# Performance work log

Measured on AMD Instinct MI355X. Metric: run time of the kernel, lower is better.

## Reference

```python
import jax, jax.numpy as jnp
import numpy as np

STATE_DIM = 150
HIDDEN = 64
ACTION_DIM = 10
TEAM = 5
PRED_STEPS = 5
HEADS = 4
BATCH = 16384


def _lin_params(key, out_dim, in_dim):
    kw, kb = jax.random.split(key)
    w = jax.random.normal(kw, (out_dim, in_dim), dtype=jnp.float32) * 0.05
    b = jax.random.normal(kb, (out_dim,), dtype=jnp.float32) * 0.05
    return w, b


def setup_inputs() -> dict:
    key = jax.random.key(0)
    ks = jax.random.split(key, 16)
    x = jax.random.normal(ks[0], (BATCH, STATE_DIM), dtype=jnp.float32)
    fc1_w, fc1_b = _lin_params(ks[1], HIDDEN, STATE_DIM)
    fc2_w, fc2_b = _lin_params(ks[2], HIDDEN, HIDDEN)
    fc3_w, fc3_b = _lin_params(ks[3], ACTION_DIM, HIDDEN)
    h0_w, h0_b = _lin_params(ks[4], HIDDEN, HIDDEN)
    c0_w, c0_b = _lin_params(ks[5], HIDDEN, HIDDEN)
    lstm_wih = jax.random.normal(ks[6], (4 * HIDDEN, HIDDEN), dtype=jnp.float32) * 0.05
    lstm_whh = jax.random.normal(ks[7], (4 * HIDDEN, HIDDEN), dtype=jnp.float32) * 0.05
    lstm_bih = jax.random.normal(ks[8], (4 * HIDDEN,), dtype=jnp.float32) * 0.05
    lstm_bhh = jax.random.normal(ks[9], (4 * HIDDEN,), dtype=jnp.float32) * 0.05
    predfc_w, predfc_b = _lin_params(ks[10], TEAM * STATE_DIM, HIDDEN)
    emb_w, emb_b = _lin_params(ks[11], HIDDEN, STATE_DIM)
    attn_in_w = jax.random.normal(ks[12], (3 * HIDDEN, HIDDEN), dtype=jnp.float32) * 0.05
    attn_in_b = jax.random.normal(ks[13], (3 * HIDDEN,), dtype=jnp.float32) * 0.05
    attn_out_w, attn_out_b = _lin_params(ks[14], HIDDEN, HIDDEN)
    unemb_w, unemb_b = _lin_params(ks[15], STATE_DIM, HIDDEN)
    return dict(x=x, fc1_w=fc1_w, fc1_b=fc1_b, fc2_w=fc2_w, fc2_b=fc2_b,
                fc3_w=fc3_w, fc3_b=fc3_b, h0_w=h0_w, h0_b=h0_b, c0_w=c0_w,
                c0_b=c0_b, lstm_wih=lstm_wih, lstm_whh=lstm_whh,
                lstm_bih=lstm_bih, lstm_bhh=lstm_bhh, predfc_w=predfc_w,
                predfc_b=predfc_b, emb_w=emb_w, emb_b=emb_b,
                attn_in_w=attn_in_w, attn_in_b=attn_in_b,
                attn_out_w=attn_out_w, attn_out_b=attn_out_b,
                unemb_w=unemb_w, unemb_b=unemb_b)


def _mha(x, in_w, in_b, out_w, out_b):
    # x: [B, S, E]; torch MultiheadAttention with batch_first=True, q=k=v=x
    B, S, E = x.shape
    D = E // HEADS
    qkv = x @ in_w.T + in_b                      # [B, S, 3E]
    q, k, v = jnp.split(qkv, 3, axis=-1)
    def heads(t):  # [B, S, E] -> [B, H, S, D]
        return t.reshape(B, S, HEADS, D).transpose(0, 2, 1, 3)
    q, k, v = heads(q), heads(k), heads(v)
    scores = jnp.einsum('bhqd,bhkd->bhqk', q, k) / jnp.sqrt(jnp.float32(D))
    attn = jax.nn.softmax(scores, axis=-1)
    out = jnp.einsum('bhqk,bhkd->bhqd', attn, v)  # [B, H, S, D]
    out = out.transpose(0, 2, 1, 3).reshape(B, S, E)
    return out @ out_w.T + out_b


def reference(x, fc1_w, fc1_b, fc2_w, fc2_b, fc3_w, fc3_b, h0_w, h0_b, c0_w,
              c0_b, lstm_wih, lstm_whh, lstm_bih, lstm_bhh, predfc_w,
              predfc_b, emb_w, emb_b, attn_in_w, attn_in_b, attn_out_w,
              attn_out_b, unemb_w, unemb_b):
    B = x.shape[0]
    h1 = jax.nn.relu(x @ fc1_w.T + fc1_b)
    h2 = jax.nn.relu(h1 @ fc2_w.T + fc2_b)
    action_probs = jax.nn.softmax(h2 @ fc3_w.T + fc3_b, axis=1)
    h = h2 @ h0_w.T + h0_b
    c = h2 @ c0_w.T + c0_b
    zero_in = jnp.zeros((B, HIDDEN), dtype=x.dtype)

    def step(carry, _):
        h, c = carry
        gates = zero_in @ lstm_wih.T + lstm_bih + h @ lstm_whh.T + lstm_bhh
        i, f, g, o = jnp.split(gates, 4, axis=-1)
        c_new = jax.nn.sigmoid(f) * c + jax.nn.sigmoid(i) * jnp.tanh(g)
        h_new = jax.nn.sigmoid(o) * jnp.tanh(c_new)
        pred_step = (h_new @ predfc_w.T + predfc_b).reshape(B, TEAM, STATE_DIM)
        embeds = pred_step @ emb_w.T + emb_b          # [B, TEAM, HIDDEN]
        att = _mha(embeds, attn_in_w, attn_in_b, attn_out_w, attn_out_b)
        out = att @ unemb_w.T + unemb_b               # [B, TEAM, STATE_DIM]
        return (h_new, c_new), out

    (_, _), preds = jax.lax.scan(step, (h, c), None, length=PRED_STEPS)
    pred = preds.transpose(1, 0, 2, 3)  # [B, PRED_STEPS, TEAM, STATE_DIM]
    return action_probs, pred
```

## Files before the change

kernel.cpp:

```cpp
#include <hip/hip_runtime.h>


#define RF(x) __builtin_amdgcn_readfirstlane(x)

constexpr int BATCH = 16384;

typedef short bf16x8 __attribute__((ext_vector_type(8)));
typedef float f32x4  __attribute__((ext_vector_type(4)));

constexpr int WS_FC1T = 0;
constexpr int WS_FC2T = 9728;
constexpr int WS_FC3T = 13824;
constexpr int WS_H0T  = 14592;
constexpr int WS_C0T  = 18688;
constexpr int WS_WHHT = 22784;
constexpr int WS_GB   = 39168;
constexpr int WS_W2   = 39424;
constexpr int WS_B2   = 59904;
constexpr int WS_W3QK = 60224;
constexpr int WS_W3V  = 101184;
constexpr int WS_B3QK = 121664;
constexpr int WS_B3V  = 122304;
constexpr int WS_W4T  = 122624;
constexpr int WS_B4   = 132352;
constexpr int WS_FC3B = 132504;
constexpr int WS_W4F  = 132520;
constexpr int WS_GF   = 142760;
constexpr int WS_VF   = 159144;
constexpr int WS_QKF  = 179624;
constexpr int WS_TOTAL= 220584;

constexpr int VSTR     = 324;
constexpr int QK_OFF   = 10368;
constexpr int QKSTR    = 164;
constexpr int H_OFF    = 15616;
constexpr int C_OFF    = 17792;
constexpr int HSTR     = 68;
constexpr int XSTR     = 156;
constexpr int H1_OFF   = QK_OFF;
constexpr int H2_OFF   = 4992;
constexpr int LDS_DW   = 19968;

__device__ __forceinline__ unsigned rnbf16_bits(float f) {
    unsigned u = __float_as_uint(f);
    return (u + 0x7FFFu + ((u >> 16) & 1u)) >> 16;
}

__global__ void k_pre1(const float* __restrict__ fc1_w, const float* __restrict__ fc2_w,
                       const float* __restrict__ fc3_w, const float* __restrict__ fc3_b,
                       const float* __restrict__ h0_w,  const float* __restrict__ c0_w,
                       const float* __restrict__ whh,   const float* __restrict__ bih,
                       const float* __restrict__ bhh,
                       const float* __restrict__ predfc_w, const float* __restrict__ predfc_b,
                       const float* __restrict__ emb_w,    const float* __restrict__ emb_b,
                       const float* __restrict__ aow, const float* __restrict__ aob,
                       const float* __restrict__ unw, const float* __restrict__ unb,
                       float* ws)
{
    int idx = blockIdx.x * 256 + threadIdx.x;
    if (idx < 9728) { int k = idx / 64, c = idx & 63;
        ws[WS_FC1T + idx] = (k < 150) ? fc1_w[c * 150 + k] : 0.f; return; }
    idx -= 9728;
    if (idx < 4096) { int k = idx >> 6, c = idx & 63; ws[WS_FC2T + idx] = fc2_w[c * 64 + k]; return; }
    idx -= 4096;
    if (idx < 768)  { int k = idx / 12, c = idx % 12;
        ws[WS_FC3T + idx] = (c < 10) ? fc3_w[c * 64 + k] : 0.f; return; }
    idx -= 768;
    if (idx < 4096) { int k = idx >> 6, c = idx & 63; ws[WS_H0T + idx] = h0_w[c * 64 + k]; return; }
    idx -= 4096;
    if (idx < 4096) { int k = idx >> 6, c = idx & 63; ws[WS_C0T + idx] = c0_w[c * 64 + k]; return; }
    idx -= 4096;
    if (idx < 16384){ int k = idx >> 8, c = idx & 255; ws[WS_WHHT + idx] = whh[c * 64 + k]; return; }
    idx -= 16384;
    if (idx < 256)  { ws[WS_GB + idx] = bih[idx] + bhh[idx]; return; }
    idx -= 256;
    if (idx < 20480){ int t = idx / 4096, r = idx & 4095, kk = r >> 6, j = r & 63;
        float s = 0.f;
        for (int m = 0; m < 150; ++m)
            s = fmaf(emb_w[kk * 150 + m], predfc_w[(t * 150 + m) * 64 + j], s);
        ws[WS_W2 + idx] = s; return; }
    idx -= 20480;
    if (idx < 320)  { int t = idx / 64, kk = idx & 63;
        float s = emb_b[kk];
        for (int m = 0; m < 150; ++m)
            s = fmaf(emb_w[kk * 150 + m], predfc_b[t * 150 + m], s);
        ws[WS_B2 + idx] = s; return; }
    idx -= 320;
    if (idx < 9728) { int k = idx / 152, ss = idx % 152;
        float v = 0.f;
        if (ss < 150) { float a = 0.f;
            for (int kk = 0; kk < 64; ++kk) a = fmaf(unw[ss * 64 + kk], aow[kk * 64 + k], a);
            v = a; }
        ws[WS_W4T + idx] = v; return; }
    idx -= 9728;
    if (idx < 152)  { float v = 0.f;
        if (idx < 150) { float a = unb[idx];
            for (int kk = 0; kk < 64; ++kk) a = fmaf(unw[idx * 64 + kk], aob[kk], a);
            v = a; }
        ws[WS_B4 + idx] = v; return; }
    idx -= 152;
    if (idx < 12)   { ws[WS_FC3B + idx] = (idx < 10) ? fc3_b[idx] : 0.f; return; }
}
constexpr int PRE1_ITEMS = 70116;

__global__ void k_pre2(const float* __restrict__ aiw, const float* __restrict__ aib,
                       float* ws)
{
    int idx = blockIdx.x * 256 + threadIdx.x;
    const float* W2 = ws + WS_W2;
    const float* b2 = ws + WS_B2;
    if (idx < 40960) {
        int h = idx / 10240, r = idx % 10240, k = r / 160, c = r % 160;
        int t = c / 32, rr = c % 32;
        int row; float scale;
        if (rr < 16) { row = h * 16 + rr;            scale = 0.25f; }
        else         { row = 64 + h * 16 + (rr - 16); scale = 1.f;  }
        float s = 0.f;
        for (int kk = 0; kk < 64; ++kk)
            s = fmaf(aiw[row * 64 + kk], W2[t * 4096 + kk * 64 + k], s);
        ws[WS_W3QK + idx] = s * scale; return;
    }
    idx -= 40960;
    if (idx < 20480) {
        int k = idx / 320, c = idx % 320, t = c >> 6, r3 = c & 63;
        int row = 128 + r3;
        float s = 0.f;
        for (int kk = 0; kk < 64; ++kk)
            s = fmaf(aiw[row * 64 + kk], W2[t * 4096 + kk * 64 + k], s);
        ws[WS_W3V + idx] = s; return;
    }
    idx -= 20480;
    if (idx < 640) {
        int h = idx / 160, c = idx % 160, t = c / 32, rr = c % 32;
        int row; float scale;
        if (rr < 16) { row = h * 16 + rr;            scale = 0.25f; }
        else         { row = 64 + h * 16 + (rr - 16); scale = 1.f;  }
        float s = aib[row];
        for (int kk = 0; kk < 64; ++kk)
            s = fmaf(aiw[row * 64 + kk], b2[t * 64 + kk], s);
        ws[WS_B3QK + idx] = s * scale; return;
    }
    idx -= 640;
    if (idx < 320) {
        int t = idx >> 6, r3 = idx & 63, row = 128 + r3;
        float s = aib[row];
        for (int kk = 0; kk < 64; ++kk)
            s = fmaf(aiw[row * 64 + kk], b2[t * 64 + kk], s);
        ws[WS_B3V + idx] = s; return;
    }
}
constexpr int PRE2_ITEMS = 62400;

__global__ void k_pre3(float* ws)
{
    int idx = blockIdx.x * 256 + threadIdx.x;
    if (idx >= 10240) return;
    int j2 = idx & 3, l = (idx >> 2) & 63, r = idx >> 8;
    int split = r & 1, s = (r >> 1) & 1, n = r >> 2;
    int col = 16 * n + (l & 15);
    unsigned bits[2];
    #pragma unroll
    for (int q = 0; q < 2; ++q) {
        int k = 32 * s + 8 * (l >> 4) + 2 * j2 + q;
        float v = (col < 152) ? ws[WS_W4T + k * 152 + col] : 0.f;
        unsigned hb = rnbf16_bits(v);
        if (split == 0) bits[q] = hb;
        else {
            float fh = __uint_as_float(hb << 16);
            bits[q] = rnbf16_bits(v - fh);
        }
    }
    reinterpret_cast<unsigned*>(ws)[WS_W4F + idx] = bits[0] | (bits[1] << 16);
}

__global__ void k_pre4(float* ws)
{
    int idx = blockIdx.x * 256 + threadIdx.x;
    if (idx >= 77824) return;
    const float* src; int N, rel, dst;
    if (idx < 16384)      { src = ws + WS_WHHT; N = 256; rel = idx;         dst = WS_GF + idx; }
    else if (idx < 36864) { src = ws + WS_W3V;  N = 320; rel = idx - 16384; dst = WS_VF + rel; }
    else {
        int r = idx - 36864;
        int h = r / 10240;  rel = r % 10240;
        src = ws + WS_W3QK + h * 10240; N = 160;
        dst = WS_QKF + r;
    }
    int n = rel >> 10, sub = rel & 1023;
    int s = sub >> 9, split = (sub >> 8) & 1, lj = sub & 255;
    int l = lj >> 2, j2 = lj & 3;
    int col = n * 16 + (l & 15);
    unsigned bits[2];
    #pragma unroll
    for (int q = 0; q < 2; ++q) {
        int k = 32 * s + 8 * (l >> 4) + 2 * j2 + q;
        float v = src[k * N + col];
        unsigned hb = rnbf16_bits(v);
        if (split == 0) bits[q] = hb;
        else bits[q] = rnbf16_bits(v - __uint_as_float(hb << 16));
    }
    reinterpret_cast<unsigned*>(ws)[dst] = bits[0] | (bits[1] << 16);
}

__device__ __forceinline__ float sigf(float v) {
    return __builtin_amdgcn_rcpf(1.f + __expf(-v));
}
__device__ __forceinline__ float tanh_fast(float v) {
    float e = __expf(-2.f * v);
    return fmaf(-2.f, e * __builtin_amdgcn_rcpf(1.f + e), 1.f);
}

template<int NC, int K, int WS>
__device__ __forceinline__ void kloop(const float* __restrict__ wT,
                                      const float* __restrict__ a_row,
                                      float* acc)
{
    #pragma unroll 4
    for (int k = 0; k < K; k += 4) {
        const float4 av = *reinterpret_cast<const float4*>(a_row + k);
        const float* wr = wT + k * WS;
        #pragma unroll
        for (int c = 0; c < NC; ++c) acc[c] = fmaf(av.x, wr[c], acc[c]);
        #pragma unroll
        for (int c = 0; c < NC; ++c) acc[c] = fmaf(av.y, wr[WS + c], acc[c]);
        #pragma unroll
        for (int c = 0; c < NC; ++c) acc[c] = fmaf(av.z, wr[2 * WS + c], acc[c]);
        #pragma unroll
        for (int c = 0; c < NC; ++c) acc[c] = fmaf(av.w, wr[3 * WS + c], acc[c]);
    }
}

__device__ __forceinline__ f32x4 mfma_tile(const bf16x8* __restrict__ base,
                                           const bf16x8* ah, const bf16x8* al,
                                           int l, f32x4 acc)
{
    #pragma unroll
    for (int s = 0; s < 2; ++s) {
        bf16x8 bh = base[s * 128 + l];
        bf16x8 bl = base[s * 128 + 64 + l];
        acc = __builtin_amdgcn_mfma_f32_16x16x32_bf16(al[s], bh, acc, 0, 0, 0);
        acc = __builtin_amdgcn_mfma_f32_16x16x32_bf16(ah[s], bl, acc, 0, 0, 0);
        acc = __builtin_amdgcn_mfma_f32_16x16x32_bf16(ah[s], bh, acc, 0, 0, 0);
    }
    return acc;
}

__device__ __forceinline__ void build_afrag(const float* __restrict__ hbase,
                                            int m, int l, bf16x8* ah, bf16x8* al)
{
    const int arow = m * 16 + (l & 15);
    const int kb   = 8 * (l >> 4);
    #pragma unroll
    for (int s = 0; s < 2; ++s) {
        const float* ap = hbase + arow * HSTR + 32 * s + kb;
        float4 f0 = *reinterpret_cast<const float4*>(ap);
        float4 f1 = *reinterpret_cast<const float4*>(ap + 4);
        float fv[8] = {f0.x, f0.y, f0.z, f0.w, f1.x, f1.y, f1.z, f1.w};
        #pragma unroll
        for (int j = 0; j < 8; ++j) {
            unsigned hb = rnbf16_bits(fv[j]);
            ah[s][j] = (short)hb;
            al[s][j] = (short)rnbf16_bits(fv[j] - __uint_as_float(hb << 16));
        }
    }
}

__global__ void __launch_bounds__(512, 2)
policy_main(const float* __restrict__ x,
            const float* __restrict__ fc1_b, const float* __restrict__ fc2_b,
            const float* __restrict__ h0_b,  const float* __restrict__ c0_b,
            const float* __restrict__ ws,    float* __restrict__ out)
{
    __shared__ float lds[LDS_DW];

    const int tid = threadIdx.x;
    const int l   = tid & 63;
    const int w   = RF(tid >> 6);
    const int m   = w & 1;
    const int g   = w >> 1;
    const int el  = l & 31;
    const int hf  = l >> 5;
    const int e0  = blockIdx.x * 32;
    const int r0c = (l >> 4) << 2;

    for (int idx = tid; idx < 32 * XSTR; idx += 512) {
        int r = idx / XSTR, k = idx - r * XSTR;
        lds[idx] = (k < 150) ? x[(e0 + r) * 150 + k] : 0.f;
    }
    __syncthreads();

    {
        const int c0 = w * 8 + hf * 4;
        float acc[4];
        #pragma unroll
        for (int c = 0; c < 4; ++c) acc[c] = fc1_b[c0 + c];
        kloop<4, 152, 64>(ws + WS_FC1T + c0, lds + el * XSTR, acc);
        float* hp = lds + H1_OFF + el * HSTR + c0;
        *reinterpret_cast<float4*>(hp) =
            make_float4(fmaxf(acc[0],0.f), fmaxf(acc[1],0.f), fmaxf(acc[2],0.f), fmaxf(acc[3],0.f));
    }
    __syncthreads();

    {
        const int c0 = w * 8 + hf * 4;
        float acc[4];
        #pragma unroll
        for (int c = 0; c < 4; ++c) acc[c] = fc2_b[c0 + c];
        kloop<4, 64, 64>(ws + WS_FC2T + c0, lds + H1_OFF + el * HSTR, acc);
        float* hp = lds + H2_OFF + el * HSTR + c0;
        *reinterpret_cast<float4*>(hp) =
            make_float4(fmaxf(acc[0],0.f), fmaxf(acc[1],0.f), fmaxf(acc[2],0.f), fmaxf(acc[3],0.f));
    }
    __syncthreads();

    if (w == 0) {
        if (hf == 0) {
            float acc[12];
            #pragma unroll
            for (int c = 0; c < 12; ++c) acc[c] = ws[WS_FC3B + c];
            kloop<12, 64, 12>(ws + WS_FC3T, lds + H2_OFF + el * HSTR, acc);
            float mm = acc[0];
            #pragma unroll
            for (int i = 1; i < 10; ++i) mm = fmaxf(mm, acc[i]);
            float sum = 0.f;
            #pragma unroll
            for (int i = 0; i < 10; ++i) { acc[i] = __expf(acc[i] - mm); sum += acc[i]; }
            float inv = __builtin_amdgcn_rcpf(sum);
            float* op = out + (size_t)(e0 + el) * 10;
            #pragma unroll
            for (int i = 0; i < 10; i += 2)
                *reinterpret_cast<float2*>(op + i) = make_float2(acc[i] * inv, acc[i + 1] * inv);
        }
    } else {
        for (int j = w - 1; j < 16; j += 7) {
            const int  cc  = (j & 7) * 8 + hf * 4;
            const bool isC = (j >= 8);
            const float* wT = ws + (isC ? WS_C0T : WS_H0T) + cc;
            const float* bb = isC ? c0_b : h0_b;
            float acc[4];
            #pragma unroll
            for (int c = 0; c < 4; ++c) acc[c] = bb[cc + c];
            kloop<4, 64, 64>(wT, lds + H2_OFF + el * HSTR, acc);
            float* dp = lds + (isC ? C_OFF : H_OFF) + el * HSTR + cc;
            *reinterpret_cast<float4*>(dp) = make_float4(acc[0], acc[1], acc[2], acc[3]);
        }
    }
    __syncthreads();

    const bf16x8* gfrag  = reinterpret_cast<const bf16x8*>(ws + WS_GF);
    const bf16x8* vfrag  = reinterpret_cast<const bf16x8*>(ws + WS_VF);
    const bf16x8* qkfrag = reinterpret_cast<const bf16x8*>(ws + WS_QKF);

    const int grp  = tid >> 5;
    const int sel  = tid & 31;
    const int team = (grp < 5) ? grp : grp - 5;
    const int half = (grp < 5) ? 0 : 1;

    #pragma unroll 1
    for (int st = 0; st < 5; ++st) {
        {
            bf16x8 ah[2], al[2];
            build_afrag(lds + H_OFF, m, l, ah, al);
            #pragma unroll 1
            for (int i = 0; i < 4; ++i) {
                const int n   = g * 4 + i;
                const int col = n * 16 + (l & 15);
                float b = ws[WS_GB + col];
                f32x4 acc = {b, b, b, b};
                acc = mfma_tile(gfrag + n * 256, ah, al, l, acc);
                #pragma unroll
                for (int q = 0; q < 4; ++q)
                    lds[(m * 16 + r0c + q) * VSTR + col] = acc[q];
            }
        }
        __syncthreads();

        {
            const int j0 = (w * 2 + hf) * 4;
            const float* gr = lds + el * VSTR;
            float* hr = lds + H_OFF + el * HSTR;
            float* cr = lds + C_OFF + el * HSTR;
            float4 ig = *reinterpret_cast<const float4*>(gr + j0);
            float4 fg = *reinterpret_cast<const float4*>(gr + 64 + j0);
            float4 gg = *reinterpret_cast<const float4*>(gr + 128 + j0);
            float4 og = *reinterpret_cast<const float4*>(gr + 192 + j0);
            float4 cv = *reinterpret_cast<const float4*>(cr + j0);
            float cn[4], hn[4];
            #pragma unroll
            for (int q = 0; q < 4; ++q) {
                float iv = (&ig.x)[q], fv = (&fg.x)[q], gv = (&gg.x)[q],
                      ov = (&og.x)[q], c_ = (&cv.x)[q];
                float cc = sigf(fv) * c_ + sigf(iv) * tanh_fast(gv);
                cn[q] = cc;
                hn[q] = sigf(ov) * tanh_fast(cc);
            }
            *reinterpret_cast<float4*>(cr + j0) = make_float4(cn[0], cn[1], cn[2], cn[3]);
            *reinterpret_cast<float4*>(hr + j0) = make_float4(hn[0], hn[1], hn[2], hn[3]);
        }
        __syncthreads();

        {
            bf16x8 ah[2], al[2];
            build_afrag(lds + H_OFF, m, l, ah, al);
            #pragma unroll 1
            for (int i = 0; i < 5; ++i) {
                const int n   = g * 5 + i;
                const int col = n * 16 + (l & 15);
                float b = ws[WS_B3V + col];
                f32x4 acc = {b, b, b, b};
                acc = mfma_tile(vfrag + n * 256, ah, al, l, acc);
                #pragma unroll
                for (int q = 0; q < 4; ++q)
                    lds[(m * 16 + r0c + q) * VSTR + col] = acc[q];
            }
            #pragma unroll 1
            for (int n = g; n < 10; n += 4) {
                const int col = n * 16 + (l & 15);
                float b = ws[WS_B3QK + col];
                f32x4 acc = {b, b, b, b};
                acc = mfma_tile(qkfrag + n * 256, ah, al, l, acc);
                #pragma unroll
                for (int q = 0; q < 4; ++q)
                    lds[QK_OFF + (m * 16 + r0c + q) * QKSTR + col] = acc[q];
            }
        }
        __syncthreads();

        float att[8];
        #pragma unroll 1
        for (int h = 0; h < 4; ++h) {
            if (tid < 320) {
                const float* qk = lds + QK_OFF + sel * QKSTR;
                float4 q0 = *reinterpret_cast<const float4*>(qk + team * 32);
                float4 q1 = *reinterpret_cast<const float4*>(qk + team * 32 + 4);
                float4 q2 = *reinterpret_cast<const float4*>(qk + team * 32 + 8);
                float4 q3 = *reinterpret_cast<const float4*>(qk + team * 32 + 12);
                float sc[5];
                #pragma unroll 2
                for (int t2 = 0; t2 < 5; ++t2) {
                    const float* kp = qk + t2 * 32 + 16;
                    float4 k0 = *reinterpret_cast<const float4*>(kp);
                    float4 k1 = *reinterpret_cast<const float4*>(kp + 4);
                    float4 k2 = *reinterpret_cast<const float4*>(kp + 8);
                    float4 k3 = *reinterpret_cast<const float4*>(kp + 12);
                    float d0 = q0.x * k0.x; d0 = fmaf(q0.y, k0.y, d0); d0 = fmaf(q0.z, k0.z, d0); d0 = fmaf(q0.w, k0.w, d0);
                    float d1 = q1.x * k1.x; d1 = fmaf(q1.y, k1.y, d1); d1 = fmaf(q1.z, k1.z, d1); d1 = fmaf(q1.w, k1.w, d1);
                    float d2 = q2.x * k2.x; d2 = fmaf(q2.y, k2.y, d2); d2 = fmaf(q2.z, k2.z, d2); d2 = fmaf(q2.w, k2.w, d2);
                    float d3 = q3.x * k3.x; d3 = fmaf(q3.y, k3.y, d3); d3 = fmaf(q3.z, k3.z, d3); d3 = fmaf(q3.w, k3.w, d3);
                    sc[t2] = (d0 + d1) + (d2 + d3);
                }
                float mm = fmaxf(fmaxf(fmaxf(sc[0], sc[1]), fmaxf(sc[2], sc[3])), sc[4]);
                float p[5];
                float sum = 0.f;
                #pragma unroll
                for (int t2 = 0; t2 < 5; ++t2) { p[t2] = __expf(sc[t2] - mm); sum += p[t2]; }
                float inv = __builtin_amdgcn_rcpf(sum);
                #pragma unroll
                for (int t2 = 0; t2 < 5; ++t2) p[t2] *= inv;

                #pragma unroll
                for (int r = 0; r < 8; ++r) att[r] = 0.f;
                const float* vr = lds + sel * VSTR + h * 16 + half * 8;
                #pragma unroll 2
                for (int t2 = 0; t2 < 5; ++t2) {
                    float4 v0 = *reinterpret_cast<const float4*>(vr + t2 * 64);
                    float4 v1 = *reinterpret_cast<const float4*>(vr + t2 * 64 + 4);
                    att[0] = fmaf(p[t2], v0.x, att[0]);
                    att[1] = fmaf(p[t2], v0.y, att[1]);
                    att[2] = fmaf(p[t2], v0.z, att[2]);
                    att[3] = fmaf(p[t2], v0.w, att[3]);
                    att[4] = fmaf(p[t2], v1.x, att[4]);
                    att[5] = fmaf(p[t2], v1.y, att[5]);
                    att[6] = fmaf(p[t2], v1.z, att[6]);
                    att[7] = fmaf(p[t2], v1.w, att[7]);
                }
            }
            __syncthreads();

            if (tid < 320) {
                float* ap = lds + sel * VSTR + team * 64 + h * 16 + half * 8;
                *reinterpret_cast<float4*>(ap)     = make_float4(att[0], att[1], att[2], att[3]);
                *reinterpret_cast<float4*>(ap + 4) = make_float4(att[4], att[5], att[6], att[7]);
            }
            if (h < 3) {
                bf16x8 ah[2], al[2];
                build_afrag(lds + H_OFF, m, l, ah, al);
                #pragma unroll 1
                for (int n = g; n < 10; n += 4) {
                    const int col = n * 16 + (l & 15);
                    float b = ws[WS_B3QK + (h + 1) * 160 + col];
                    f32x4 acc = {b, b, b, b};
                    acc = mfma_tile(qkfrag + (h + 1) * 2560 + n * 256, ah, al, l, acc);
                    #pragma unroll
                    for (int q = 0; q < 4; ++q)
                        lds[QK_OFF + (m * 16 + r0c + q) * QKSTR + col] = acc[q];
                }
            }
            __syncthreads();
        }

        #pragma unroll 1
        for (int job = w; job < 10; job += 8) {
            const int t  = job >> 1;
            const int mj = job & 1;
            const int arow  = mj * 16 + (l & 15);
            const int kbase = 8 * (l >> 4);
            bf16x8 ah[2], al[2];
            #pragma unroll
            for (int s = 0; s < 2; ++s) {
                const float* ap = lds + arow * VSTR + t * 64 + 32 * s + kbase;
                float4 f0 = *reinterpret_cast<const float4*>(ap);
                float4 f1 = *reinterpret_cast<const float4*>(ap + 4);
                float fv[8] = {f0.x, f0.y, f0.z, f0.w, f1.x, f1.y, f1.z, f1.w};
                #pragma unroll
                for (int j = 0; j < 8; ++j) {
                    unsigned hb = rnbf16_bits(fv[j]);
                    float fh = __uint_as_float(hb << 16);
                    ah[s][j] = (short)hb;
                    al[s][j] = (short)rnbf16_bits(fv[j] - fh);
                }
            }
            const bf16x8* wb = reinterpret_cast<const bf16x8*>(ws + WS_W4F);
            const int cl = l & 15;
            #pragma unroll 1
            for (int n = 0; n < 10; ++n) {
                const int c = n * 16 + cl;
                float bias = ws[WS_B4 + (c < 151 ? c : 151)];
                f32x4 acc = {bias, bias, bias, bias};
                acc = mfma_tile(wb + n * 256, ah, al, l, acc);
                if (c < 150) {
                    const int r0 = mj * 16 + r0c;
                    #pragma unroll
                    for (int q = 0; q < 4; ++q)
                        out[(size_t)BATCH * 10 +
                            ((size_t)((e0 + r0 + q) * 5 + st) * 5 + t) * 150 + c] = acc[q];
                }
            }
        }
        __syncthreads();
    }
}

extern "C" void kernel_launch(void* const* d_in, const int* in_sizes, int n_in,
                              void* d_out, int out_size, void* d_ws, size_t ws_size,
                              hipStream_t stream)
{
    const float* x        = (const float*)d_in[0];
    const float* fc1_w    = (const float*)d_in[1];
    const float* fc1_b    = (const float*)d_in[2];
    const float* fc2_w    = (const float*)d_in[3];
    const float* fc2_b    = (const float*)d_in[4];
    const float* fc3_w    = (const float*)d_in[5];
    const float* fc3_b    = (const float*)d_in[6];
    const float* h0_w     = (const float*)d_in[7];
    const float* h0_b     = (const float*)d_in[8];
    const float* c0_w     = (const float*)d_in[9];
    const float* c0_b     = (const float*)d_in[10];
    const float* lstm_whh = (const float*)d_in[12];
    const float* lstm_bih = (const float*)d_in[13];
    const float* lstm_bhh = (const float*)d_in[14];
    const float* predfc_w = (const float*)d_in[15];
    const float* predfc_b = (const float*)d_in[16];
    const float* emb_w    = (const float*)d_in[17];
    const float* emb_b    = (const float*)d_in[18];
    const float* attn_in_w= (const float*)d_in[19];
    const float* attn_in_b= (const float*)d_in[20];
    const float* attn_out_w=(const float*)d_in[21];
    const float* attn_out_b=(const float*)d_in[22];
    const float* unemb_w  = (const float*)d_in[23];
    const float* unemb_b  = (const float*)d_in[24];

    float* ws  = (float*)d_ws;
    float* outp= (float*)d_out;

    k_pre1<<<(PRE1_ITEMS + 255) / 256, 256, 0, stream>>>(
        fc1_w, fc2_w, fc3_w, fc3_b, h0_w, c0_w,
        lstm_whh, lstm_bih, lstm_bhh,
        predfc_w, predfc_b, emb_w, emb_b,
        attn_out_w, attn_out_b, unemb_w, unemb_b, ws);

    k_pre2<<<(PRE2_ITEMS + 255) / 256, 256, 0, stream>>>(attn_in_w, attn_in_b, ws);

    k_pre3<<<40, 256, 0, stream>>>(ws);
    k_pre4<<<304, 256, 0, stream>>>(ws);

    policy_main<<<BATCH / 32, 512, 0, stream>>>(
        x, fc1_b, fc2_b, h0_b, c0_b, ws, outp);
}
```

Baseline: 230.0 us.

## Fuse LSTM gate MFMA with cell update in registers and hoist h fragment

Each wave now computes the i,f,g,o gate tiles for the same hidden column and applies the LSTM cell update directly from the MFMA accumulators. This removes the gate round-trip through LDS and one barrier per prediction step. The bf16 hi/lo fragments of the new h are built once per step and reused for the V, QK and later-head projections instead of being rebuilt each time. The cost is more live accumulator and fragment registers, which could hurt occupancy.

```diff
diff --git a/kernel.cpp b/kernel.cpp
--- a/kernel.cpp
+++ b/kernel.cpp
@@ -355,53 +355,36 @@
     const int sel  = tid & 31;
     const int team = (grp < 5) ? grp : grp - 5;
     const int half = (grp < 5) ? 0 : 1;
+    const int jcol = g * 16 + (l & 15);
 
     #pragma unroll 1
     for (int st = 0; st < 5; ++st) {
         {
             bf16x8 ah[2], al[2];
             build_afrag(lds + H_OFF, m, l, ah, al);
+            f32x4 gacc[4];
             #pragma unroll 1
-            for (int i = 0; i < 4; ++i) {
-                const int n   = g * 4 + i;
-                const int col = n * 16 + (l & 15);
-                float b = ws[WS_GB + col];
+            for (int gi = 0; gi < 4; ++gi) {
+                const int n = gi * 4 + g;
+                float b = ws[WS_GB + gi * 64 + jcol];
                 f32x4 acc = {b, b, b, b};
-                acc = mfma_tile(gfrag + n * 256, ah, al, l, acc);
-                #pragma unroll
-                for (int q = 0; q < 4; ++q)
-                    lds[(m * 16 + r0c + q) * VSTR + col] = acc[q];
+                gacc[gi] = mfma_tile(gfrag + n * 256, ah, al, l, acc);
+            }
+            #pragma unroll
+            for (int q = 0; q < 4; ++q) {
+                const int row = m * 16 + r0c + q;
+                float c_ = lds[C_OFF + row * HSTR + jcol];
+                float cc = sigf(gacc[1][q]) * c_ + sigf(gacc[0][q]) * tanh_fast(gacc[2][q]);
+                float hn = sigf(gacc[3][q]) * tanh_fast(cc);
+                lds[C_OFF + row * HSTR + jcol] = cc;
+                lds[H_OFF + row * HSTR + jcol] = hn;
             }
         }
         __syncthreads();
 
+        bf16x8 ah[2], al[2];
+        build_afrag(lds + H_OFF, m, l, ah, al);
         {
-            const int j0 = (w * 2 + hf) * 4;
-            const float* gr = lds + el * VSTR;
-            float* hr = lds + H_OFF + el * HSTR;
-            float* cr = lds + C_OFF + el * HSTR;
-            float4 ig = *reinterpret_cast<const float4*>(gr + j0);
-            float4 fg = *reinterpret_cast<const float4*>(gr + 64 + j0);
-            float4 gg = *reinterpret_cast<const float4*>(gr + 128 + j0);
-            float4 og = *reinterpret_cast<const float4*>(gr + 192 + j0);
-            float4 cv = *reinterpret_cast<const float4*>(cr + j0);
-            float cn[4], hn[4];
-            #pragma unroll
-            for (int q = 0; q < 4; ++q) {
-                float iv = (&ig.x)[q], fv = (&fg.x)[q], gv = (&gg.x)[q],
-                      ov = (&og.x)[q], c_ = (&cv.x)[q];
-                float cc = sigf(fv) * c_ + sigf(iv) * tanh_fast(gv);
-                cn[q] = cc;
-                hn[q] = sigf(ov) * tanh_fast(cc);
-            }
-            *reinterpret_cast<float4*>(cr + j0) = make_float4(cn[0], cn[1], cn[2], cn[3]);
-            *reinterpret_cast<float4*>(hr + j0) = make_float4(hn[0], hn[1], hn[2], hn[3]);
-        }
-        __syncthreads();
-
-        {
-            bf16x8 ah[2], al[2];
-            build_afrag(lds + H_OFF, m, l, ah, al);
             #pragma unroll 1
             for (int i = 0; i < 5; ++i) {
                 const int n   = g * 5 + i;
@@ -483,8 +466,6 @@
                 *reinterpret_cast<float4*>(ap + 4) = make_float4(att[4], att[5], att[6], att[7]);
             }
             if (h < 3) {
-                bf16x8 ah[2], al[2];
-                build_afrag(lds + H_OFF, m, l, ah, al);
                 #pragma unroll 1
                 for (int n = g; n < 10; n += 4) {
                     const int col = n * 16 + (l & 15);
@@ -505,7 +486,7 @@
             const int mj = job & 1;
             const int arow  = mj * 16 + (l & 15);
             const int kbase = 8 * (l >> 4);
-            bf16x8 ah[2], al[2];
+            bf16x8 ah2[2], al2[2];
             #pragma unroll
             for (int s = 0; s < 2; ++s) {
                 const float* ap = lds + arow * VSTR + t * 64 + 32 * s + kbase;
@@ -516,8 +497,8 @@
                 for (int j = 0; j < 8; ++j) {
                     unsigned hb = rnbf16_bits(fv[j]);
                     float fh = __uint_as_float(hb << 16);
-                    ah[s][j] = (short)hb;
-                    al[s][j] = (short)rnbf16_bits(fv[j] - fh);
+                    ah2[s][j] = (short)hb;
+                    al2[s][j] = (short)rnbf16_bits(fv[j] - fh);
                 }
             }
             const bf16x8* wb = reinterpret_cast<const bf16x8*>(ws + WS_W4F);
@@ -527,7 +508,7 @@
                 const int c = n * 16 + cl;
                 float bias = ws[WS_B4 + (c < 151 ? c : 151)];
                 f32x4 acc = {bias, bias, bias, bias};
-                acc = mfma_tile(wb + n * 256, ah, al, l, acc);
+                acc = mfma_tile(wb + n * 256, ah2, al2, l, acc);
                 if (c < 150) {
                     const int r0 = mj * 16 + r0c;
                     #pragma unroll
```

After: 228.0 us. About the same (-0.9%).
